# Kernel tuning notes

Hardware: AMD Instinct MI355X
Metric: run time of the kernel (lower is better)

Reference implementation:

```python
import jax, jax.numpy as jnp
import numpy as np

POOL = (2, 2, 2)   # LPPool3d kernel == stride
KH, KW = 3, 3      # unfold kernel
EPS = 1e-6


def setup_inputs() -> dict:
    key = jax.random.key(0)
    k1, k2, k3 = jax.random.split(key, 3)
    x = jax.random.normal(k1, (32, 8, 4, 256, 256), dtype=jnp.float32)
    patch_dim = 8 * (4 // POOL[0]) * KH * KW  # 144
    out_dim = 128
    lin_w = jax.random.normal(k2, (out_dim, patch_dim), dtype=jnp.float32) * (1.0 / np.sqrt(patch_dim))
    lin_b = jax.random.normal(k3, (out_dim,), dtype=jnp.float32) * 0.01
    return {"x": x, "lin_w": lin_w, "lin_b": lin_b}


def reference(x, lin_w, lin_b):
    N, C, D, H, W = x.shape
    kd, kh, kw = POOL
    # LPPool3d with p=2, stride==kernel: (sum of squares in window)^(1/2)
    xr = (x * x).reshape(N, C, D // kd, kd, H // kh, kh, W // kw, kw)
    pooled = jnp.sqrt(xr.sum(axis=(3, 5, 7)))  # (N, C, Dp, Hp, Wp)
    Dp, Hp, Wp = pooled.shape[2], pooled.shape[3], pooled.shape[4]
    # merge depth into channels: permute(0,2,1,3,4).view(N, Dp*C, Hp, Wp)
    merged = pooled.transpose(0, 2, 1, 3, 4).reshape(N, Dp * C, Hp, Wp)
    MC = Dp * C
    Ho, Wo = Hp - KH + 1, Wp - KW + 1
    # im2col matching torch.nn.Unfold ordering: (channel, kh, kw) flattened
    slices = [merged[:, :, i:i + Ho, j:j + Wo] for i in range(KH) for j in range(KW)]
    patches = jnp.stack(slices, axis=2)                 # (N, MC, KH*KW, Ho, Wo)
    patches = patches.reshape(N, MC * KH * KW, Ho * Wo) # (N, patch_dim, L)
    patches = patches.transpose(0, 2, 1)                # (N, L, patch_dim)
    # per-patch linear + CELU (alpha=1)
    proj = jnp.einsum('nlk,ok->nlo', patches, lin_w) + lin_b  # (N, L, out_dim)
    act = jax.nn.celu(proj)
    # aggregate over patches, then L2-normalize with clamped norm
    agg = act.mean(axis=1)                              # (N, out_dim)
    norm = jnp.maximum(jnp.linalg.norm(agg, axis=1, keepdims=True), EPS)
    return agg / norm
```

## Files before the change

### kernel.cpp

```cpp
#include <hip/hip_runtime.h>
#include <math.h>

#define NB   32
#define C    8
#define D    4
#define H    256
#define W    256
#define HP   128
#define WP   128
#define MC   16
#define HO   126
#define WO   126
#define PATCH 144
#define OUTD 128
#define NL   (HO*WO)
#define HOG  6
#define NGRP (HO/HOG)
#define PROWS 9
#define BROW 168

typedef float  f32x4  __attribute__((ext_vector_type(4)));
typedef __bf16 bf16x8 __attribute__((ext_vector_type(8)));

__global__ __launch_bounds__(256, 2)
void fused_kernel(const float* __restrict__ x, const float* __restrict__ lin_w,
                  const float* __restrict__ lin_b, float* __restrict__ accg) {
    __shared__ __align__(16) char smem[PROWS*128*32 + OUTD*BROW*2];
    __bf16* Pl   = (__bf16*)smem;
    __bf16* Blds = (__bf16*)(smem + PROWS*128*32);

    int blk = blockIdx.x;
    int g = blk % NGRP, n = blk / NGRP;
    int ho0 = g * HOG;
    int t = threadIdx.x;
    int wave = t >> 6, lane = t & 63, quad = lane >> 4, l16 = lane & 15;

    {
        int wp = t & 127, dph = t >> 7;
        const float* xn = x + (size_t)n * (C*D*H*W);
#pragma unroll 2
        for (int i = 0; i < 8; i++) {
            int hp = ho0 + i;
            bf16x8 pk;
#pragma unroll
            for (int c = 0; c < 8; c++) {
                const float* xb = xn + ((c*4 + 2*dph) * H + 2*hp) * W + 2*wp;
                float2 a0 = *(const float2*)(xb);
                float2 a1 = *(const float2*)(xb + W);
                float2 a2 = *(const float2*)(xb + H*W);
                float2 a3 = *(const float2*)(xb + H*W + W);
                float s = a0.x*a0.x + a0.y*a0.y + a1.x*a1.x + a1.y*a1.y
                        + a2.x*a2.x + a2.y*a2.y + a3.x*a3.x + a3.y*a3.y;
                pk[c] = (__bf16)sqrtf(s);
            }
            *(bf16x8*)&Pl[(i*128 + wp)*16 + dph*8] = pk;
        }
        bf16x8 z = {};
        *(bf16x8*)&Pl[(8*128 + wp)*16 + dph*8] = z;
    }

    {
        int o = t & 127, kh = t >> 7;
#pragma unroll 4
        for (int kk = 0; kk < 80; kk++) {
            int kn = kh*80 + kk;
            int tap = kn >> 4, mc = kn & 15;
            float v = (tap < 9) ? lin_w[o*PATCH + mc*9 + tap] : 0.f;
            Blds[o*BROW + kn] = (__bf16)v;
        }
    }

    float lb[8];
#pragma unroll
    for (int nt = 0; nt < 8; nt++) lb[nt] = lin_b[nt*16 + l16];

    __syncthreads();

    float srun[8] = {0,0,0,0,0,0,0,0};
    int h8 = (quad & 1) * 8;
    int m0 = wave * 32 + l16;

    for (int hh = 0; hh < HOG; hh++) {
        f32x4 acc[2][8] = {};
#pragma unroll
        for (int ks = 0; ks < 5; ks++) {
            int tap = 2*ks + (quad >> 1);
            int it = (tap * 11) >> 5;
            int jt = tap - it * 3;
            bf16x8 afr[2];
#pragma unroll
            for (int mt = 0; mt < 2; mt++) {
                int m = m0 + mt*16;
                afr[mt] = *(const bf16x8*)&Pl[((hh + it)*128 + m + jt)*16 + h8];
            }
#pragma unroll
            for (int nt = 0; nt < 8; nt++) {
                bf16x8 bfr = *(const bf16x8*)&Blds[(nt*16 + l16)*BROW + ks*32 + quad*8];
                acc[0][nt] = __builtin_amdgcn_mfma_f32_16x16x32_bf16(afr[0], bfr, acc[0][nt], 0, 0, 0);
                acc[1][nt] = __builtin_amdgcn_mfma_f32_16x16x32_bf16(afr[1], bfr, acc[1][nt], 0, 0, 0);
            }
        }
#pragma unroll
        for (int nt = 0; nt < 8; nt++) {
            float s = 0.f;
#pragma unroll
            for (int mt = 0; mt < 2; mt++) {
                int mb = wave*32 + mt*16 + quad*4;
#pragma unroll
                for (int r = 0; r < 4; r++) {
                    float p = acc[mt][nt][r] + lb[nt];
                    float a = (p > 0.f) ? p : (__expf(p) - 1.f);
                    if (mb + r < WO) s += a;
                }
            }
            s += __shfl_xor(s, 16, 64);
            s += __shfl_xor(s, 32, 64);
            srun[nt] += s;
        }
    }

    __syncthreads();
    float* red = (float*)smem;
    if (quad == 0) {
#pragma unroll
        for (int nt = 0; nt < 8; nt++) red[wave*OUTD + nt*16 + l16] = srun[nt];
    }
    __syncthreads();
    if (t < OUTD) {
        float tot = red[t] + red[OUTD+t] + red[2*OUTD+t] + red[3*OUTD+t];
        atomicAdd(&accg[n*OUTD + t], tot);
    }
}

__global__ void finalize_kernel(const float* __restrict__ acc, float* __restrict__ out) {
    int n = blockIdx.x;
    int o = threadIdx.x;
    float a = acc[n * OUTD + o] * (1.0f / (float)NL);
    float s = a * a;
#pragma unroll
    for (int off = 32; off > 0; off >>= 1) s += __shfl_down(s, off, 64);
    __shared__ float partial[2];
    if ((o & 63) == 0) partial[o >> 6] = s;
    __syncthreads();
    float norm = sqrtf(partial[0] + partial[1]);
    norm = fmaxf(norm, 1e-6f);
    out[n * OUTD + o] = a / norm;
}

extern "C" void kernel_launch(void* const* d_in, const int* in_sizes, int n_in,
                              void* d_out, int out_size, void* d_ws, size_t ws_size,
                              hipStream_t stream) {
    const float* x     = (const float*)d_in[0];
    const float* lin_w = (const float*)d_in[1];
    const float* lin_b = (const float*)d_in[2];
    float* out = (float*)d_out;

    float* acc = (float*)d_ws;

    hipMemsetAsync(acc, 0, NB * OUTD * sizeof(float), stream);
    fused_kernel<<<NB * NGRP, 256, 0, stream>>>(x, lin_w, lin_b, acc);
    finalize_kernel<<<NB, OUTD, 0, stream>>>(acc, out);
}
```

Baseline: 432.8 us.

## Split LP-pool into separate kernel writing bf16 merged map to workspace

Moves the LP pooling out of the fused GEMM kernel into its own kernel that writes a bf16 pooled tensor to workspace. The GEMM kernel then copies pooled rows from global memory into LDS. This removes the 8/6 redundant recomputation of overlapping pooled rows across row-groups and gives the memory-bound pooling pass high occupancy. The cost is an extra kernel launch and a global round trip for the intermediate. The change also shrinks the padded weight row width and replaces the branch in the masked CELU sum with a multiply by a precomputed mask.

Measured after the change: 449.1 us. +3.8%, slower.

```diff
diff --git a/kernel.cpp b/kernel.cpp
--- a/kernel.cpp
+++ b/kernel.cpp
@@ -2,10 +2,10 @@
 #include <math.h>
 
 #define NB   32
-#define C    8
-#define D    4
-#define H    256
-#define W    256
+#define C_   8
+#define D_   4
+#define H_   256
+#define W_   256
 #define HP   128
 #define WP   128
 #define MC   16
@@ -16,18 +16,43 @@
 #define NL   (HO*WO)
 #define HOG  6
 #define NGRP (HO/HOG)
-#define PROWS 9
-#define BROW 168
+#define BROW 160
 
 typedef float  f32x4  __attribute__((ext_vector_type(4)));
 typedef __bf16 bf16x8 __attribute__((ext_vector_type(8)));
 
+__global__ __launch_bounds__(256, 8) void pool_kernel(const float* __restrict__ x,
+                                                      __bf16* __restrict__ merged) {
+    int t  = threadIdx.x;
+    int wp = t & 127;
+    int hp = (blockIdx.x & 63) * 2 + (t >> 7);
+    int n  = blockIdx.x >> 6;
+
+    const float* xb = x + (size_t)n * (C_*D_*H_*W_) + 2*hp*W_ + 2*wp;
+    bf16x8 lo, hi;
+#pragma unroll
+    for (int mc = 0; mc < 16; mc++) {
+        int dp = mc >> 3, c = mc & 7;
+        const float* p = xb + (size_t)(c*4 + 2*dp) * (H_*W_);
+        float2 a0 = *(const float2*)(p);
+        float2 a1 = *(const float2*)(p + W_);
+        float2 a2 = *(const float2*)(p + H_*W_);
+        float2 a3 = *(const float2*)(p + H_*W_ + W_);
+        float s = a0.x*a0.x + a0.y*a0.y + a1.x*a1.x + a1.y*a1.y
+                + a2.x*a2.x + a2.y*a2.y + a3.x*a3.x + a3.y*a3.y;
+        if (mc < 8) lo[mc] = (__bf16)sqrtf(s); else hi[mc-8] = (__bf16)sqrtf(s);
+    }
+    __bf16* dst = merged + (((size_t)n*HP + hp)*WP + wp) * MC;
+    *(bf16x8*)dst       = lo;
+    *(bf16x8*)(dst + 8) = hi;
+}
+
 __global__ __launch_bounds__(256, 2)
-void fused_kernel(const float* __restrict__ x, const float* __restrict__ lin_w,
-                  const float* __restrict__ lin_b, float* __restrict__ accg) {
-    __shared__ __align__(16) char smem[PROWS*128*32 + OUTD*BROW*2];
+void gemm_kernel(const __bf16* __restrict__ merged, const float* __restrict__ lin_w,
+                 const float* __restrict__ lin_b, float* __restrict__ accg) {
+    __shared__ __align__(16) char smem[9*128*32 + OUTD*BROW*2];
     __bf16* Pl   = (__bf16*)smem;
-    __bf16* Blds = (__bf16*)(smem + PROWS*128*32);
+    __bf16* Blds = (__bf16*)(smem + 9*128*32);
 
     int blk = blockIdx.x;
     int g = blk % NGRP, n = blk / NGRP;
@@ -36,34 +61,19 @@
     int wave = t >> 6, lane = t & 63, quad = lane >> 4, l16 = lane & 15;
 
     {
-        int wp = t & 127, dph = t >> 7;
-        const float* xn = x + (size_t)n * (C*D*H*W);
-#pragma unroll 2
-        for (int i = 0; i < 8; i++) {
-            int hp = ho0 + i;
-            bf16x8 pk;
+        const __bf16* msrc = merged + ((size_t)n*HP + ho0) * WP * MC;
 #pragma unroll
-            for (int c = 0; c < 8; c++) {
-                const float* xb = xn + ((c*4 + 2*dph) * H + 2*hp) * W + 2*wp;
-                float2 a0 = *(const float2*)(xb);
-                float2 a1 = *(const float2*)(xb + W);
-                float2 a2 = *(const float2*)(xb + H*W);
-                float2 a3 = *(const float2*)(xb + H*W + W);
-                float s = a0.x*a0.x + a0.y*a0.y + a1.x*a1.x + a1.y*a1.y
-                        + a2.x*a2.x + a2.y*a2.y + a3.x*a3.x + a3.y*a3.y;
-                pk[c] = (__bf16)sqrtf(s);
-            }
-            *(bf16x8*)&Pl[(i*128 + wp)*16 + dph*8] = pk;
-        }
+        for (int i = 0; i < 8; i++)
+            *(bf16x8*)&Pl[i*2048 + t*8] = *(const bf16x8*)&msrc[i*2048 + t*8];
         bf16x8 z = {};
-        *(bf16x8*)&Pl[(8*128 + wp)*16 + dph*8] = z;
+        *(bf16x8*)&Pl[8*2048 + t*8] = z;
     }
 
     {
         int o = t & 127, kh = t >> 7;
 #pragma unroll 4
-        for (int kk = 0; kk < 80; kk++) {
-            int kn = kh*80 + kk;
+        for (int kk = 0; kk < BROW/2; kk++) {
+            int kn = kh*(BROW/2) + kk;
             int tap = kn >> 4, mc = kn & 15;
             float v = (tap < 9) ? lin_w[o*PATCH + mc*9 + tap] : 0.f;
             Blds[o*BROW + kn] = (__bf16)v;
@@ -73,6 +83,13 @@
     float lb[8];
 #pragma unroll
     for (int nt = 0; nt < 8; nt++) lb[nt] = lin_b[nt*16 + l16];
+
+    float msk[2][4];
+#pragma unroll
+    for (int mt = 0; mt < 2; mt++)
+#pragma unroll
+        for (int r = 0; r < 4; r++)
+            msk[mt][r] = (wave*32 + mt*16 + quad*4 + r < WO) ? 1.f : 0.f;
 
     __syncthreads();
 
@@ -105,12 +122,11 @@
             float s = 0.f;
 #pragma unroll
             for (int mt = 0; mt < 2; mt++) {
-                int mb = wave*32 + mt*16 + quad*4;
 #pragma unroll
                 for (int r = 0; r < 4; r++) {
                     float p = acc[mt][nt][r] + lb[nt];
                     float a = (p > 0.f) ? p : (__expf(p) - 1.f);
-                    if (mb + r < WO) s += a;
+                    s += msk[mt][r] * a;
                 }
             }
             s += __shfl_xor(s, 16, 64);
@@ -155,9 +171,12 @@
     const float* lin_b = (const float*)d_in[2];
     float* out = (float*)d_out;
 
-    float* acc = (float*)d_ws;
+    float*  acc    = (float*)d_ws;
+    __bf16* merged = (__bf16*)((char*)d_ws + NB*OUTD*4);
 
     hipMemsetAsync(acc, 0, NB * OUTD * sizeof(float), stream);
-    fused_kernel<<<NB * NGRP, 256, 0, stream>>>(x, lin_w, lin_b, acc);
+
+    pool_kernel<<<NB * 64, 256, 0, stream>>>(x, merged);
+    gemm_kernel<<<NB * NGRP, 256, 0, stream>>>(merged, lin_w, lin_b, acc);
     finalize_kernel<<<NB, OUTD, 0, stream>>>(acc, out);
 }
```
